# Kernel tuning notes

Measured on AMD Instinct MI355X. Metric: run time of the kernel, lower is better.

The kernel has to match this reference:

```python
import jax, jax.numpy as jnp
import numpy as np

N_HEAD = 16
N_FEAT = 1024
D_K = N_FEAT // N_HEAD


def rtt_half(x):
    x1, x2 = x[..., : x.shape[-1] // 2], x[..., x.shape[-1] // 2 :]
    return jnp.concatenate([-x2, x1], axis=-1)


def setup_inputs() -> dict:
    key = jax.random.key(0)
    ks = jax.random.split(key, 16)
    B, T, D = 4, 2048, N_FEAT
    inp = {
        "query": jax.random.normal(ks[0], (B, T, D), jnp.float32),
        "key": jax.random.normal(ks[1], (B, T, D), jnp.float32),
        "value": jax.random.normal(ks[2], (B, T, D), jnp.float32),
        "cos": jax.random.uniform(ks[3], (T, 1, D_K), jnp.float32),
        "sin": jax.random.uniform(ks[4], (T, 1, D_K), jnp.float32),
        "mask": jnp.zeros((B, T, T), jnp.bool_),
    }
    s = 1.0 / np.sqrt(D)
    inp["Wq"] = jax.random.uniform(ks[5], (D, D), jnp.float32, -s, s)
    inp["bq"] = jax.random.uniform(ks[6], (D,), jnp.float32, -s, s)
    inp["Wk"] = jax.random.uniform(ks[7], (D, D), jnp.float32, -s, s)
    inp["bk"] = jax.random.uniform(ks[8], (D,), jnp.float32, -s, s)
    inp["Wv"] = jax.random.uniform(ks[9], (D, D), jnp.float32, -s, s)
    inp["bv"] = jax.random.uniform(ks[10], (D,), jnp.float32, -s, s)
    inp["Wo"] = jax.random.uniform(ks[11], (D, D), jnp.float32, -s, s)
    inp["bo"] = jax.random.uniform(ks[12], (D,), jnp.float32, -s, s)
    return inp


def reference(query, key, value, cos, sin, mask, Wq, bq, Wk, bk, Wv, bv, Wo, bo):
    B, T, D = query.shape
    h, d_k = N_HEAD, D_K
    # QKV projections (torch Linear: x @ W.T + b), reshape to (B,T,h,d_k)
    q = (query @ Wq.T + bq).reshape(B, T, h, d_k)
    k = (key @ Wk.T + bk).reshape(B, T, h, d_k)
    v = (value @ Wv.T + bv).reshape(B, T, h, d_k)
    # RoPE: cos/sin sliced to T, broadcast (T,1,d_k) over (B,T,h,d_k)
    c, s = cos[:T], sin[:T]
    q = q * c + rtt_half(q) * s
    k = k * c + rtt_half(k) * s
    # attention scores (B,h,T,T)
    scores = jnp.einsum("bqhd,bkhd->bhqk", q, k) / np.sqrt(d_k).astype(jnp.float32)
    scores = jnp.where(mask[:, None, :, :], -jnp.inf, scores)
    attn = jax.nn.softmax(scores, axis=-1)
    out = jnp.einsum("bhqk,bkhd->bqhd", attn, v).reshape(B, T, D)
    return out @ Wo.T + bo
```

## Files before the change

kernel.cpp:

```cpp
#include <hip/hip_runtime.h>

#define B_SZ 4
#define T_SZ 2048
#define D_SZ 1024
#define H_SZ 16
#define DK_SZ 64
#define M_SZ (B_SZ * T_SZ)

typedef __attribute__((ext_vector_type(8))) short bf16x8;
typedef __attribute__((ext_vector_type(4))) short bf16x4;
typedef __attribute__((ext_vector_type(4))) float f32x4;

union fui { float f; unsigned u; };

static __device__ inline short f2bf(float x) {
    union { float f; unsigned u; } v; v.f = x;
    unsigned r = v.u + 0x7fff + ((v.u >> 16) & 1);
    return (short)(r >> 16);
}
static __device__ inline void split1(float f, short* h, short* l) {
    fui a; a.f = f;
    *h = (short)(a.u >> 16);
    fui t; t.u = a.u & 0xffff0000u;
    fui r; r.f = f - t.f;
    *l = (short)(r.u >> 16);
}

#define MFMA16(a, b, c) __builtin_amdgcn_mfma_f32_16x16x32_bf16((a), (b), (c), 0, 0, 0)

#define GLDS16(g, l) __builtin_amdgcn_global_load_lds(                        \
    (const __attribute__((address_space(1))) unsigned int*)(g),               \
    (__attribute__((address_space(3))) unsigned int*)(l), 16, 0, 0)

static __device__ inline void split8(float4 f0, float4 f1, bf16x8* hi, bf16x8* lo)
{
    fui a[8];
    a[0].f = f0.x; a[1].f = f0.y; a[2].f = f0.z; a[3].f = f0.w;
    a[4].f = f1.x; a[5].f = f1.y; a[6].f = f1.z; a[7].f = f1.w;
    union { unsigned w[4]; bf16x8 v; } H, L;
#pragma unroll
    for (int p = 0; p < 4; ++p)
        H.w[p] = __builtin_amdgcn_perm(a[2 * p + 1].u, a[2 * p].u, 0x07060302);
#pragma unroll
    for (int j = 0; j < 8; ++j) {
        fui t; t.u = a[j].u & 0xffff0000u;
        fui r; r.f = a[j].f - t.f;
        a[j].u = r.u;
    }
#pragma unroll
    for (int p = 0; p < 4; ++p)
        L.w[p] = __builtin_amdgcn_perm(a[2 * p + 1].u, a[2 * p].u, 0x07060302);
    *hi = H.v; *lo = L.v;
}

__global__ __launch_bounds__(256)
void wsplit_kernel(const float* __restrict__ W, short* __restrict__ Wh,
                   short* __restrict__ Wl)
{
    const int i = blockIdx.x * 256 + threadIdx.x;
    float4 f = ((const float4*)W)[i];
    fui a[4]; a[0].f = f.x; a[1].f = f.y; a[2].f = f.z; a[3].f = f.w;
    union { short s[4]; short4 v; } H, L;
#pragma unroll
    for (int j = 0; j < 4; ++j) {
        H.s[j] = (short)(a[j].u >> 16);
        fui t; t.u = a[j].u & 0xffff0000u;
        fui r; r.f = a[j].f - t.f;
        L.s[j] = (short)(r.u >> 16);
    }
    ((short4*)Wh)[i] = H.v;
    ((short4*)Wl)[i] = L.v;
}

__global__ __launch_bounds__(256)
void mask_flags_kernel(const unsigned char* __restrict__ mask, int* __restrict__ flags)
{
    const int f = blockIdx.x * 4 + (threadIdx.x >> 6);
    const int lane = threadIdx.x & 63;
    const int b = f >> 10, qt = (f >> 5) & 31, kt = f & 31;
    const unsigned char* base = mask + ((size_t)b * T_SZ + qt * 64) * T_SZ + kt * 64;
    bool nz = false;
#pragma unroll
    for (int i = 0; i < 4; ++i) {
        const int c = lane + 64 * i;
        const int row = c >> 2, off = (c & 3) * 16;
        uint4 v = *(const uint4*)(base + (size_t)row * T_SZ + off);
        nz |= ((v.x | v.y | v.z | v.w) != 0);
    }
    unsigned long long bal = __ballot(nz);
    if (lane == 0) flags[f] = (bal != 0) ? 1 : 0;
}

__global__ __launch_bounds__(256)
void qkv_mfma_kernel(const float* __restrict__ Aq, const float* __restrict__ Ak,
                     const float* __restrict__ Av,
                     const short* __restrict__ Wqh, const short* __restrict__ Wql,
                     const short* __restrict__ Wkh, const short* __restrict__ Wkl,
                     const short* __restrict__ Wvh, const short* __restrict__ Wvl,
                     const float* __restrict__ bq, const float* __restrict__ bk,
                     const float* __restrict__ bv,
                     const float* __restrict__ cosb, const float* __restrict__ sinb,
                     short* __restrict__ Qh, short* __restrict__ Ql,
                     short* __restrict__ Kh, short* __restrict__ Kl,
                     short* __restrict__ Vb)
{
    __shared__ __align__(16) short Whs[128 * 32];
    __shared__ __align__(16) short Wls[128 * 32];

    const int which = blockIdx.y >> 3;
    const int m0 = blockIdx.x * 128, n0 = (blockIdx.y & 7) * 128;
    const float* A  = (which == 0) ? Aq  : (which == 1) ? Ak  : Av;
    const short* Wh = (which == 0) ? Wqh : (which == 1) ? Wkh : Wvh;
    const short* Wl = (which == 0) ? Wql : (which == 1) ? Wkl : Wvl;
    const float* bias = (which == 0) ? bq : (which == 1) ? bk : bv;

    const int tid = threadIdx.x;
    const int wv = tid >> 6, lane = tid & 63;
    const int wm = wv >> 1, wn = wv & 1;
    const int l15 = lane & 15, quad = lane >> 4;

    f32x4 acc[4][4];
#pragma unroll
    for (int mt = 0; mt < 4; ++mt)
#pragma unroll
        for (int nt = 0; nt < 4; ++nt)
            acc[mt][nt] = (f32x4){0.f, 0.f, 0.f, 0.f};

    const short* whg = Wh + (size_t)(n0 + wv * 32 + (lane >> 2)) * D_SZ + (lane & 3) * 8;
    const short* wlg = Wl + (size_t)(n0 + wv * 32 + (lane >> 2)) * D_SZ + (lane & 3) * 8;
    short* whl0 = &Whs[wv * 1024];
    short* wll0 = &Wls[wv * 1024];

    const float* aB[4];
#pragma unroll
    for (int mt = 0; mt < 4; ++mt)
        aB[mt] = A + (size_t)(m0 + wm * 64 + mt * 16 + l15) * D_SZ + quad * 8;

    for (int k0 = 0; k0 < D_SZ; k0 += 32) {
        float4 af0[4], af1[4];
#pragma unroll
        for (int mt = 0; mt < 4; ++mt) {
            af0[mt] = *(const float4*)(aB[mt] + k0);
            af1[mt] = *(const float4*)(aB[mt] + k0 + 4);
        }
        __syncthreads();
        GLDS16(whg + k0,             whl0);
        GLDS16(whg + 16 * D_SZ + k0, whl0 + 512);
        GLDS16(wlg + k0,             wll0);
        GLDS16(wlg + 16 * D_SZ + k0, wll0 + 512);

        bf16x8 ah[4], al[4];
#pragma unroll
        for (int mt = 0; mt < 4; ++mt)
            split8(af0[mt], af1[mt], &ah[mt], &al[mt]);

        __syncthreads();

#pragma unroll
        for (int nt = 0; nt < 4; ++nt) {
            const int brow = (wn * 64 + nt * 16 + l15) * 32 + quad * 8;
            const bf16x8 bh = *(const bf16x8*)&Whs[brow];
            const bf16x8 bl = *(const bf16x8*)&Wls[brow];
#pragma unroll
            for (int mt = 0; mt < 4; ++mt) {
                acc[mt][nt] = MFMA16(ah[mt], bh, acc[mt][nt]);
                acc[mt][nt] = MFMA16(al[mt], bh, acc[mt][nt]);
                acc[mt][nt] = MFMA16(ah[mt], bl, acc[mt][nt]);
            }
        }
    }

    const int hh = ((blockIdx.y & 7) << 1) + wn;
    if (which < 2) {
        short* Hd = (which == 0) ? Qh : Kh;
        short* Ld = (which == 0) ? Ql : Kl;
        const float qscale = (which == 0) ? 0.125f : 1.0f;
#pragma unroll
        for (int mt = 0; mt < 4; ++mt)
#pragma unroll
            for (int p = 0; p < 2; ++p) {
                const int d1 = p * 16 + l15, d2 = d1 + 32;
                const int col1 = n0 + wn * 64 + d1;
                const float b1 = bias[col1], b2 = bias[col1 + 32];
#pragma unroll
                for (int r = 0; r < 4; ++r) {
                    const int m = m0 + wm * 64 + mt * 16 + quad * 4 + r;
                    const int bb = m >> 11, tg = m & (T_SZ - 1);
                    const float c1 = cosb[tg * 64 + d1], s1 = sinb[tg * 64 + d1];
                    const float c2 = cosb[tg * 64 + d2], s2 = sinb[tg * 64 + d2];
                    const float x1 = acc[mt][p][r] + b1;
                    const float x2 = acc[mt][p + 2][r] + b2;
                    const float y1 = (x1 * c1 - x2 * s1) * qscale;
                    const float y2 = (x2 * c2 + x1 * s2) * qscale;
                    const size_t base = (((size_t)(bb * H_SZ + hh)) * T_SZ + tg) * 64;
                    short h_, l_;
                    split1(y1, &h_, &l_); Hd[base + d1] = h_; Ld[base + d1] = l_;
                    split1(y2, &h_, &l_); Hd[base + d2] = h_; Ld[base + d2] = l_;
                }
            }
    } else {
#pragma unroll
        for (int nt = 0; nt < 4; ++nt) {
            const int d = nt * 16 + l15;
            const float bvv = bias[n0 + wn * 64 + d];
#pragma unroll
            for (int mt = 0; mt < 4; ++mt)
#pragma unroll
                for (int r = 0; r < 4; ++r) {
                    const int m = m0 + wm * 64 + mt * 16 + quad * 4 + r;
                    const int bb = m >> 11, tg = m & (T_SZ - 1);
                    Vb[(((size_t)(bb * H_SZ + hh)) * T_SZ + tg) * 64 + d] =
                        f2bf(acc[mt][nt][r] + bvv);
                }
        }
    }
}

__global__ __launch_bounds__(256)
void gemm_out_kernel(const float* __restrict__ A, const short* __restrict__ Wh,
                     const short* __restrict__ Wl, const float* __restrict__ bias,
                     float* __restrict__ C)
{
    __shared__ __align__(16) short Whs[128 * 32];
    __shared__ __align__(16) short Wls[128 * 32];

    const int m0 = blockIdx.x * 128, n0 = blockIdx.y * 128;
    const int tid = threadIdx.x;
    const int wv = tid >> 6, lane = tid & 63;
    const int wm = wv >> 1, wn = wv & 1;
    const int l15 = lane & 15, quad = lane >> 4;

    f32x4 acc[4][4];
#pragma unroll
    for (int mt = 0; mt < 4; ++mt)
#pragma unroll
        for (int nt = 0; nt < 4; ++nt)
            acc[mt][nt] = (f32x4){0.f, 0.f, 0.f, 0.f};

    const short* whg = Wh + (size_t)(n0 + wv * 32 + (lane >> 2)) * D_SZ + (lane & 3) * 8;
    const short* wlg = Wl + (size_t)(n0 + wv * 32 + (lane >> 2)) * D_SZ + (lane & 3) * 8;
    short* whl0 = &Whs[wv * 1024];
    short* wll0 = &Wls[wv * 1024];

    const float* aB[4];
#pragma unroll
    for (int mt = 0; mt < 4; ++mt)
        aB[mt] = A + (size_t)(m0 + wm * 64 + mt * 16 + l15) * D_SZ + quad * 8;

    for (int k0 = 0; k0 < D_SZ; k0 += 32) {
        float4 af0[4], af1[4];
#pragma unroll
        for (int mt = 0; mt < 4; ++mt) {
            af0[mt] = *(const float4*)(aB[mt] + k0);
            af1[mt] = *(const float4*)(aB[mt] + k0 + 4);
        }
        __syncthreads();
        GLDS16(whg + k0,             whl0);
        GLDS16(whg + 16 * D_SZ + k0, whl0 + 512);
        GLDS16(wlg + k0,             wll0);
        GLDS16(wlg + 16 * D_SZ + k0, wll0 + 512);

        bf16x8 ah[4], al[4];
#pragma unroll
        for (int mt = 0; mt < 4; ++mt)
            split8(af0[mt], af1[mt], &ah[mt], &al[mt]);

        __syncthreads();

#pragma unroll
        for (int nt = 0; nt < 4; ++nt) {
            const int brow = (wn * 64 + nt * 16 + l15) * 32 + quad * 8;
            const bf16x8 bh = *(const bf16x8*)&Whs[brow];
            const bf16x8 bl = *(const bf16x8*)&Wls[brow];
#pragma unroll
            for (int mt = 0; mt < 4; ++mt) {
                acc[mt][nt] = MFMA16(ah[mt], bh, acc[mt][nt]);
                acc[mt][nt] = MFMA16(al[mt], bh, acc[mt][nt]);
                acc[mt][nt] = MFMA16(ah[mt], bl, acc[mt][nt]);
            }
        }
    }

#pragma unroll
    for (int nt = 0; nt < 4; ++nt) {
        const int col = n0 + wn * 64 + nt * 16 + l15;
        const float bvv = bias[col];
#pragma unroll
        for (int mt = 0; mt < 4; ++mt)
#pragma unroll
            for (int r = 0; r < 4; ++r) {
                const int m = m0 + wm * 64 + mt * 16 + quad * 4 + r;
                C[(size_t)m * D_SZ + col] = acc[mt][nt][r] + bvv;
            }
    }
}

__global__ __launch_bounds__(256)
void attn_mfma_kernel(const short* __restrict__ Qhg, const short* __restrict__ Qlg,
                      const short* __restrict__ Khg, const short* __restrict__ Klg,
                      const short* __restrict__ Vg,
                      const unsigned char* __restrict__ mask,
                      const int* __restrict__ flags,
                      float* __restrict__ ob)
{
    __shared__ __align__(16) short Khs[64 * 72];
    __shared__ __align__(16) short Kls[64 * 72];
    __shared__ __align__(16) short Vt[64 * 72];
    __shared__ __align__(16) short Ps[4 * 16 * 72];

    const int bh = blockIdx.y;
    const int b = bh >> 4, h = bh & 15;
    const int q0 = blockIdx.x * 64;
    const int tid = threadIdx.x;
    const int wv = tid >> 6, lane = tid & 63;
    const int l15 = lane & 15, quad = lane >> 4;

    const short* qhp = Qhg + ((size_t)bh * T_SZ + q0 + wv * 16 + l15) * 64 + quad * 8;
    const short* qlp = Qlg + ((size_t)bh * T_SZ + q0 + wv * 16 + l15) * 64 + quad * 8;
    bf16x8 qh[2], ql[2];
#pragma unroll
    for (int s = 0; s < 2; ++s) {
        qh[s] = *(const bf16x8*)(qhp + 32 * s);
        ql[s] = *(const bf16x8*)(qlp + 32 * s);
    }

    f32x4 accO[4];
#pragma unroll
    for (int nt = 0; nt < 4; ++nt) accO[nt] = (f32x4){0.f, 0.f, 0.f, 0.f};
    float m_i[4], l_i[4];
#pragma unroll
    for (int r = 0; r < 4; ++r) { m_i[r] = -1e30f; l_i[r] = 0.f; }

    const short* khb = Khg + (size_t)bh * T_SZ * 64;
    const short* klb = Klg + (size_t)bh * T_SZ * 64;
    const short* vb  = Vg  + (size_t)bh * T_SZ * 64;
    const unsigned char* mbase = mask + ((size_t)b * T_SZ + q0) * T_SZ;
    const int* frow = flags + ((size_t)b * 32 + blockIdx.x) * 32;

    const short* kgp[4];
    short*       kld[4];
#pragma unroll
    for (int jj = 0; jj < 4; ++jj) {
        const int cc = tid + 256 * (jj & 1);
        const int row = cc >> 3, off = (cc & 7) * 8;
        kgp[jj] = ((jj < 2) ? khb : klb) + (size_t)row * 64 + off;
        kld[jj] = ((jj < 2) ? Khs : Kls) + row * 72 + off;
    }
    const int vt0 = (tid & 15) * 4, vd0 = (tid >> 4) * 4;
    const short* vgp[4];
#pragma unroll
    for (int i = 0; i < 4; ++i)
        vgp[i] = vb + (size_t)(vt0 + i) * 64 + vd0;
    short* pw = &Ps[wv * 16 * 72];

    bf16x8 kst[4];
    uint2  rv[4];
#pragma unroll
    for (int jj = 0; jj < 4; ++jj) kst[jj] = *(const bf16x8*)(kgp[jj]);
#pragma unroll
    for (int i = 0; i < 4; ++i)    rv[i]   = *(const uint2*)(vgp[i]);

    for (int kti = 0; kti < 32; ++kti) {
        const int kt = kti * 64;
        __syncthreads();
#pragma unroll
        for (int jj = 0; jj < 4; ++jj)
            *(bf16x8*)kld[jj] = kst[jj];
#pragma unroll
        for (int c = 0; c < 4; ++c) {
            const int k = c >> 1;
            const unsigned sel = (c & 1) ? 0x07060302u : 0x05040100u;
            const unsigned lo0 = k ? rv[0].y : rv[0].x;
            const unsigned lo1 = k ? rv[1].y : rv[1].x;
            const unsigned lo2 = k ? rv[2].y : rv[2].x;
            const unsigned lo3 = k ? rv[3].y : rv[3].x;
            uint2 o;
            o.x = __builtin_amdgcn_perm(lo1, lo0, sel);
            o.y = __builtin_amdgcn_perm(lo3, lo2, sel);
            *(uint2*)&Vt[(vd0 + c) * 72 + vt0] = o;
        }
        if (kti < 31) {
            const size_t adv = (size_t)(kt + 64) * 64;
#pragma unroll
            for (int jj = 0; jj < 4; ++jj)
                kst[jj] = *(const bf16x8*)(kgp[jj] + adv);
#pragma unroll
            for (int i = 0; i < 4; ++i)
                rv[i] = *(const uint2*)(vgp[i] + adv);
        }
        __syncthreads();

        f32x4 accS[4];
        __builtin_amdgcn_s_setprio(1);
#pragma unroll
        for (int nt = 0; nt < 4; ++nt) {
            f32x4 acc = (f32x4){0.f, 0.f, 0.f, 0.f};
#pragma unroll
            for (int s = 0; s < 2; ++s) {
                const bf16x8 kh = *(const bf16x8*)&Khs[(nt * 16 + l15) * 72 + 32 * s + quad * 8];
                const bf16x8 kl = *(const bf16x8*)&Kls[(nt * 16 + l15) * 72 + 32 * s + quad * 8];
                acc = MFMA16(qh[s], kh, acc);
                acc = MFMA16(ql[s], kh, acc);
                acc = MFMA16(qh[s], kl, acc);
            }
            accS[nt] = acc;
        }
        __builtin_amdgcn_s_setprio(0);

        float sv[4][4];
        if (frow[kti]) {
#pragma unroll
            for (int nt = 0; nt < 4; ++nt)
#pragma unroll
                for (int r = 0; r < 4; ++r) {
                    const unsigned char mb =
                        mbase[(size_t)(wv * 16 + quad * 4 + r) * T_SZ + kt + nt * 16 + l15];
                    sv[nt][r] = mb ? -1e30f : accS[nt][r];
                }
        } else {
#pragma unroll
            for (int nt = 0; nt < 4; ++nt)
#pragma unroll
                for (int r = 0; r < 4; ++r)
                    sv[nt][r] = accS[nt][r];
        }

        float rmax[4];
#pragma unroll
        for (int r = 0; r < 4; ++r)
            rmax[r] = fmaxf(fmaxf(sv[0][r], sv[1][r]), fmaxf(sv[2][r], sv[3][r]));
#pragma unroll
        for (int off = 1; off < 16; off <<= 1)
#pragma unroll
            for (int r = 0; r < 4; ++r)
                rmax[r] = fmaxf(rmax[r], __shfl_xor(rmax[r], off, 64));

        float alpha[4];
#pragma unroll
        for (int r = 0; r < 4; ++r) {
            const float mnew = fmaxf(m_i[r], rmax[r]);
            alpha[r] = __expf(m_i[r] - mnew);
            m_i[r] = mnew;
        }
        float lsum[4] = {0.f, 0.f, 0.f, 0.f};
#pragma unroll
        for (int nt = 0; nt < 4; ++nt)
#pragma unroll
            for (int r = 0; r < 4; ++r) {
                const float p = __expf(sv[nt][r] - m_i[r]);
                sv[nt][r] = p;
                lsum[r] += p;
            }
#pragma unroll
        for (int r = 0; r < 4; ++r)
            l_i[r] = l_i[r] * alpha[r] + lsum[r];

#pragma unroll
        for (int nt = 0; nt < 4; ++nt)
#pragma unroll
            for (int r = 0; r < 4; ++r) {
                fui u; u.f = sv[nt][r];
                pw[(quad * 4 + r) * 72 + nt * 16 + l15] = (short)((u.u + 0x8000u) >> 16);
            }

#pragma unroll
        for (int nt = 0; nt < 4; ++nt)
#pragma unroll
            for (int r = 0; r < 4; ++r)
                accO[nt][r] *= alpha[r];

        bf16x8 pa[2];
#pragma unroll
        for (int s = 0; s < 2; ++s)
            pa[s] = *(const bf16x8*)&pw[l15 * 72 + 32 * s + quad * 8];
        __builtin_amdgcn_s_setprio(1);
#pragma unroll
        for (int nt = 0; nt < 4; ++nt)
#pragma unroll
            for (int s = 0; s < 2; ++s) {
                const bf16x8 vf = *(const bf16x8*)&Vt[(nt * 16 + l15) * 72 + 32 * s + quad * 8];
                accO[nt] = MFMA16(pa[s], vf, accO[nt]);
            }
        __builtin_amdgcn_s_setprio(0);
    }

#pragma unroll
    for (int off = 1; off < 16; off <<= 1)
#pragma unroll
        for (int r = 0; r < 4; ++r)
            l_i[r] += __shfl_xor(l_i[r], off, 64);

#pragma unroll
    for (int r = 0; r < 4; ++r) {
        const float inv = 1.f / l_i[r];
        const int t = q0 + wv * 16 + quad * 4 + r;
        float* orow = ob + ((size_t)(b * T_SZ + t)) * D_SZ + h * DK_SZ;
#pragma unroll
        for (int nt = 0; nt < 4; ++nt)
            orow[nt * 16 + l15] = accO[nt][r] * inv;
    }
}

extern "C" void kernel_launch(void* const* d_in, const int* in_sizes, int n_in,
                              void* d_out, int out_size, void* d_ws, size_t ws_size,
                              hipStream_t stream)
{
    const float* query = (const float*)d_in[0];
    const float* key   = (const float*)d_in[1];
    const float* value = (const float*)d_in[2];
    const float* cosb  = (const float*)d_in[3];
    const float* sinb  = (const float*)d_in[4];
    const unsigned char* mask = (const unsigned char*)d_in[5];
    const float* Wq = (const float*)d_in[6];
    const float* bq = (const float*)d_in[7];
    const float* Wk = (const float*)d_in[8];
    const float* bk = (const float*)d_in[9];
    const float* Wv = (const float*)d_in[10];
    const float* bv = (const float*)d_in[11];
    const float* Wo = (const float*)d_in[12];
    const float* bo = (const float*)d_in[13];
    float* out = (float*)d_out;

    short* sp = (short*)d_ws;
    const size_t eb = (size_t)B_SZ * H_SZ * T_SZ * DK_SZ;
    short* Qh = sp;          short* Ql = sp + eb;
    short* Kh = sp + 2 * eb; short* Kl = sp + 3 * eb;
    short* Vb = sp + 4 * eb;
    float* abuf = (float*)(sp + 5 * eb);
    short* wsp = (short*)(abuf + eb);
    const size_t wlen = (size_t)D_SZ * D_SZ;
    short* wqh = wsp;            short* wql = wsp + wlen;
    short* wkh = wsp + 2 * wlen; short* wkl = wsp + 3 * wlen;
    short* wvh = wsp + 4 * wlen; short* wvl = wsp + 5 * wlen;
    short* woh = wsp + 6 * wlen; short* wol = wsp + 7 * wlen;
    int* flags = (int*)(wsp + 8 * wlen);

    const int wsBlocks = (int)(wlen / 4 / 256);
    wsplit_kernel<<<wsBlocks, 256, 0, stream>>>(Wq, wqh, wql);
    wsplit_kernel<<<wsBlocks, 256, 0, stream>>>(Wk, wkh, wkl);
    wsplit_kernel<<<wsBlocks, 256, 0, stream>>>(Wv, wvh, wvl);
    wsplit_kernel<<<wsBlocks, 256, 0, stream>>>(Wo, woh, wol);

    mask_flags_kernel<<<1024, 256, 0, stream>>>(mask, flags);

    qkv_mfma_kernel<<<dim3(M_SZ / 128, 24), 256, 0, stream>>>(
        query, key, value, wqh, wql, wkh, wkl, wvh, wvl,
        bq, bk, bv, cosb, sinb, Qh, Ql, Kh, Kl, Vb);

    attn_mfma_kernel<<<dim3(T_SZ / 64, B_SZ * H_SZ), 256, 0, stream>>>(
        Qh, Ql, Kh, Kl, Vb, mask, flags, abuf);

    gemm_out_kernel<<<dim3(M_SZ / 128, D_SZ / 128), 256, 0, stream>>>(
        abuf, woh, wol, bo, out);
}
```

Baseline: 728.6 us.

## Pre-split GEMM activations to bf16 hi/lo and stage them via LDS

After: 665.5 us. 8.7% less time.

```diff
diff --git a/kernel.cpp b/kernel.cpp
--- a/kernel.cpp
+++ b/kernel.cpp
@@ -31,27 +31,6 @@
 #define GLDS16(g, l) __builtin_amdgcn_global_load_lds(                        \
     (const __attribute__((address_space(1))) unsigned int*)(g),               \
     (__attribute__((address_space(3))) unsigned int*)(l), 16, 0, 0)
-
-static __device__ inline void split8(float4 f0, float4 f1, bf16x8* hi, bf16x8* lo)
-{
-    fui a[8];
-    a[0].f = f0.x; a[1].f = f0.y; a[2].f = f0.z; a[3].f = f0.w;
-    a[4].f = f1.x; a[5].f = f1.y; a[6].f = f1.z; a[7].f = f1.w;
-    union { unsigned w[4]; bf16x8 v; } H, L;
-#pragma unroll
-    for (int p = 0; p < 4; ++p)
-        H.w[p] = __builtin_amdgcn_perm(a[2 * p + 1].u, a[2 * p].u, 0x07060302);
-#pragma unroll
-    for (int j = 0; j < 8; ++j) {
-        fui t; t.u = a[j].u & 0xffff0000u;
-        fui r; r.f = a[j].f - t.f;
-        a[j].u = r.u;
-    }
-#pragma unroll
-    for (int p = 0; p < 4; ++p)
-        L.w[p] = __builtin_amdgcn_perm(a[2 * p + 1].u, a[2 * p].u, 0x07060302);
-    *hi = H.v; *lo = L.v;
-}
 
 __global__ __launch_bounds__(256)
 void wsplit_kernel(const float* __restrict__ W, short* __restrict__ Wh,
@@ -92,28 +71,19 @@
 }
 
 __global__ __launch_bounds__(256)
-void qkv_mfma_kernel(const float* __restrict__ Aq, const float* __restrict__ Ak,
-                     const float* __restrict__ Av,
-                     const short* __restrict__ Wqh, const short* __restrict__ Wql,
-                     const short* __restrict__ Wkh, const short* __restrict__ Wkl,
-                     const short* __restrict__ Wvh, const short* __restrict__ Wvl,
-                     const float* __restrict__ bq, const float* __restrict__ bk,
-                     const float* __restrict__ bv,
+void qkv_mfma_kernel(const short* __restrict__ Ah, const short* __restrict__ Al,
+                     const short* __restrict__ Wh, const short* __restrict__ Wl,
+                     const float* __restrict__ bias,
                      const float* __restrict__ cosb, const float* __restrict__ sinb,
-                     short* __restrict__ Qh, short* __restrict__ Ql,
-                     short* __restrict__ Kh, short* __restrict__ Kl,
-                     short* __restrict__ Vb)
+                     short* __restrict__ Hd, short* __restrict__ Ld,
+                     short* __restrict__ Vb, const int which)
 {
+    __shared__ __align__(16) short Ahs[128 * 32];
+    __shared__ __align__(16) short Als[128 * 32];
     __shared__ __align__(16) short Whs[128 * 32];
     __shared__ __align__(16) short Wls[128 * 32];
 
-    const int which = blockIdx.y >> 3;
-    const int m0 = blockIdx.x * 128, n0 = (blockIdx.y & 7) * 128;
-    const float* A  = (which == 0) ? Aq  : (which == 1) ? Ak  : Av;
-    const short* Wh = (which == 0) ? Wqh : (which == 1) ? Wkh : Wvh;
-    const short* Wl = (which == 0) ? Wql : (which == 1) ? Wkl : Wvl;
-    const float* bias = (which == 0) ? bq : (which == 1) ? bk : bv;
-
+    const int m0 = blockIdx.x * 128, n0 = blockIdx.y * 128;
     const int tid = threadIdx.x;
     const int wv = tid >> 6, lane = tid & 63;
     const int wm = wv >> 1, wn = wv & 1;
@@ -126,36 +96,36 @@
         for (int nt = 0; nt < 4; ++nt)
             acc[mt][nt] = (f32x4){0.f, 0.f, 0.f, 0.f};
 
-    const short* whg = Wh + (size_t)(n0 + wv * 32 + (lane >> 2)) * D_SZ + (lane & 3) * 8;
-    const short* wlg = Wl + (size_t)(n0 + wv * 32 + (lane >> 2)) * D_SZ + (lane & 3) * 8;
-    short* whl0 = &Whs[wv * 1024];
-    short* wll0 = &Wls[wv * 1024];
-
-    const float* aB[4];
-#pragma unroll
-    for (int mt = 0; mt < 4; ++mt)
-        aB[mt] = A + (size_t)(m0 + wm * 64 + mt * 16 + l15) * D_SZ + quad * 8;
+    const size_t aoff = (size_t)(m0 + wv * 32 + (lane >> 2)) * D_SZ + (lane & 3) * 8;
+    const size_t woff = (size_t)(n0 + wv * 32 + (lane >> 2)) * D_SZ + (lane & 3) * 8;
+    const short* ahg = Ah + aoff;
+    const short* alg = Al + aoff;
+    const short* whg = Wh + woff;
+    const short* wlg = Wl + woff;
+    short* ah0 = &Ahs[wv * 1024];
+    short* al0 = &Als[wv * 1024];
+    short* wh0 = &Whs[wv * 1024];
+    short* wl0 = &Wls[wv * 1024];
 
     for (int k0 = 0; k0 < D_SZ; k0 += 32) {
-        float4 af0[4], af1[4];
+        __syncthreads();
+        GLDS16(ahg + k0,             ah0);
+        GLDS16(ahg + 16 * D_SZ + k0, ah0 + 512);
+        GLDS16(alg + k0,             al0);
+        GLDS16(alg + 16 * D_SZ + k0, al0 + 512);
+        GLDS16(whg + k0,             wh0);
+        GLDS16(whg + 16 * D_SZ + k0, wh0 + 512);
+        GLDS16(wlg + k0,             wl0);
+        GLDS16(wlg + 16 * D_SZ + k0, wl0 + 512);
+        __syncthreads();
+
+        bf16x8 ah[4], al[4];
 #pragma unroll
         for (int mt = 0; mt < 4; ++mt) {
-            af0[mt] = *(const float4*)(aB[mt] + k0);
-            af1[mt] = *(const float4*)(aB[mt] + k0 + 4);
-        }
-        __syncthreads();
-        GLDS16(whg + k0,             whl0);
-        GLDS16(whg + 16 * D_SZ + k0, whl0 + 512);
-        GLDS16(wlg + k0,             wll0);
-        GLDS16(wlg + 16 * D_SZ + k0, wll0 + 512);
-
-        bf16x8 ah[4], al[4];
-#pragma unroll
-        for (int mt = 0; mt < 4; ++mt)
-            split8(af0[mt], af1[mt], &ah[mt], &al[mt]);
-
-        __syncthreads();
-
+            const int arow = (wm * 64 + mt * 16 + l15) * 32 + quad * 8;
+            ah[mt] = *(const bf16x8*)&Ahs[arow];
+            al[mt] = *(const bf16x8*)&Als[arow];
+        }
 #pragma unroll
         for (int nt = 0; nt < 4; ++nt) {
             const int brow = (wn * 64 + nt * 16 + l15) * 32 + quad * 8;
@@ -170,10 +140,8 @@
         }
     }
 
-    const int hh = ((blockIdx.y & 7) << 1) + wn;
+    const int hh = (blockIdx.y << 1) + wn;
     if (which < 2) {
-        short* Hd = (which == 0) ? Qh : Kh;
-        short* Ld = (which == 0) ? Ql : Kl;
         const float qscale = (which == 0) ? 0.125f : 1.0f;
 #pragma unroll
         for (int mt = 0; mt < 4; ++mt)
@@ -217,10 +185,12 @@
 }
 
 __global__ __launch_bounds__(256)
-void gemm_out_kernel(const float* __restrict__ A, const short* __restrict__ Wh,
-                     const short* __restrict__ Wl, const float* __restrict__ bias,
-                     float* __restrict__ C)
+void gemm_out_kernel(const short* __restrict__ Ah, const short* __restrict__ Al,
+                     const short* __restrict__ Wh, const short* __restrict__ Wl,
+                     const float* __restrict__ bias, float* __restrict__ C)
 {
+    __shared__ __align__(16) short Ahs[128 * 32];
+    __shared__ __align__(16) short Als[128 * 32];
     __shared__ __align__(16) short Whs[128 * 32];
     __shared__ __align__(16) short Wls[128 * 32];
 
@@ -237,36 +207,36 @@
         for (int nt = 0; nt < 4; ++nt)
             acc[mt][nt] = (f32x4){0.f, 0.f, 0.f, 0.f};
 
-    const short* whg = Wh + (size_t)(n0 + wv * 32 + (lane >> 2)) * D_SZ + (lane & 3) * 8;
-    const short* wlg = Wl + (size_t)(n0 + wv * 32 + (lane >> 2)) * D_SZ + (lane & 3) * 8;
-    short* whl0 = &Whs[wv * 1024];
-    short* wll0 = &Wls[wv * 1024];
-
-    const float* aB[4];
-#pragma unroll
-    for (int mt = 0; mt < 4; ++mt)
-        aB[mt] = A + (size_t)(m0 + wm * 64 + mt * 16 + l15) * D_SZ + quad * 8;
+    const size_t aoff = (size_t)(m0 + wv * 32 + (lane >> 2)) * D_SZ + (lane & 3) * 8;
+    const size_t woff = (size_t)(n0 + wv * 32 + (lane >> 2)) * D_SZ + (lane & 3) * 8;
+    const short* ahg = Ah + aoff;
+    const short* alg = Al + aoff;
+    const short* whg = Wh + woff;
+    const short* wlg = Wl + woff;
+    short* ah0 = &Ahs[wv * 1024];
+    short* al0 = &Als[wv * 1024];
+    short* wh0 = &Whs[wv * 1024];
+    short* wl0 = &Wls[wv * 1024];
 
     for (int k0 = 0; k0 < D_SZ; k0 += 32) {
-        float4 af0[4], af1[4];
+        __syncthreads();
+        GLDS16(ahg + k0,             ah0);
+        GLDS16(ahg + 16 * D_SZ + k0, ah0 + 512);
+        GLDS16(alg + k0,             al0);
+        GLDS16(alg + 16 * D_SZ + k0, al0 + 512);
+        GLDS16(whg + k0,             wh0);
+        GLDS16(whg + 16 * D_SZ + k0, wh0 + 512);
+        GLDS16(wlg + k0,             wl0);
+        GLDS16(wlg + 16 * D_SZ + k0, wl0 + 512);
+        __syncthreads();
+
+        bf16x8 ah[4], al[4];
 #pragma unroll
         for (int mt = 0; mt < 4; ++mt) {
-            af0[mt] = *(const float4*)(aB[mt] + k0);
-            af1[mt] = *(const float4*)(aB[mt] + k0 + 4);
-        }
-        __syncthreads();
-        GLDS16(whg + k0,             whl0);
-        GLDS16(whg + 16 * D_SZ + k0, whl0 + 512);
-        GLDS16(wlg + k0,             wll0);
-        GLDS16(wlg + 16 * D_SZ + k0, wll0 + 512);
-
-        bf16x8 ah[4], al[4];
-#pragma unroll
-        for (int mt = 0; mt < 4; ++mt)
-            split8(af0[mt], af1[mt], &ah[mt], &al[mt]);
-
-        __syncthreads();
-
+            const int arow = (wm * 64 + mt * 16 + l15) * 32 + quad * 8;
+            ah[mt] = *(const bf16x8*)&Ahs[arow];
+            al[mt] = *(const bf16x8*)&Als[arow];
+        }
 #pragma unroll
         for (int nt = 0; nt < 4; ++nt) {
             const int brow = (wn * 64 + nt * 16 + l15) * 32 + quad * 8;
@@ -301,7 +271,7 @@
                       const short* __restrict__ Vg,
                       const unsigned char* __restrict__ mask,
                       const int* __restrict__ flags,
-                      float* __restrict__ ob)
+                      short* __restrict__ Oh, short* __restrict__ Ol)
 {
     __shared__ __align__(16) short Khs[64 * 72];
     __shared__ __align__(16) short Kls[64 * 72];
@@ -494,10 +464,14 @@
     for (int r = 0; r < 4; ++r) {
         const float inv = 1.f / l_i[r];
         const int t = q0 + wv * 16 + quad * 4 + r;
-        float* orow = ob + ((size_t)(b * T_SZ + t)) * D_SZ + h * DK_SZ;
-#pragma unroll
-        for (int nt = 0; nt < 4; ++nt)
-            orow[nt * 16 + l15] = accO[nt][r] * inv;
+        const size_t base = ((size_t)(b * T_SZ + t)) * D_SZ + h * DK_SZ;
+#pragma unroll
+        for (int nt = 0; nt < 4; ++nt) {
+            short h_, l_;
+            split1(accO[nt][r] * inv, &h_, &l_);
+            Oh[base + nt * 16 + l15] = h_;
+            Ol[base + nt * 16 + l15] = l_;
+        }
     }
 }
 
@@ -526,8 +500,8 @@
     short* Qh = sp;          short* Ql = sp + eb;
     short* Kh = sp + 2 * eb; short* Kl = sp + 3 * eb;
     short* Vb = sp + 4 * eb;
-    float* abuf = (float*)(sp + 5 * eb);
-    short* wsp = (short*)(abuf + eb);
+    short* Xh = sp + 5 * eb; short* Xl = sp + 6 * eb;
+    short* wsp = sp + 7 * eb;
     const size_t wlen = (size_t)D_SZ * D_SZ;
     short* wqh = wsp;            short* wql = wsp + wlen;
     short* wkh = wsp + 2 * wlen; short* wkl = wsp + 3 * wlen;
@@ -536,6 +510,7 @@
     int* flags = (int*)(wsp + 8 * wlen);
 
     const int wsBlocks = (int)(wlen / 4 / 256);
+    const int aBlocks  = (int)((size_t)M_SZ * D_SZ / 4 / 256);
     wsplit_kernel<<<wsBlocks, 256, 0, stream>>>(Wq, wqh, wql);
     wsplit_kernel<<<wsBlocks, 256, 0, stream>>>(Wk, wkh, wkl);
     wsplit_kernel<<<wsBlocks, 256, 0, stream>>>(Wv, wvh, wvl);
@@ -543,13 +518,19 @@
 
     mask_flags_kernel<<<1024, 256, 0, stream>>>(mask, flags);
 
-    qkv_mfma_kernel<<<dim3(M_SZ / 128, 24), 256, 0, stream>>>(
-        query, key, value, wqh, wql, wkh, wkl, wvh, wvl,
-        bq, bk, bv, cosb, sinb, Qh, Ql, Kh, Kl, Vb);
+    wsplit_kernel<<<aBlocks, 256, 0, stream>>>(query, Xh, Xl);
+    qkv_mfma_kernel<<<dim3(M_SZ / 128, 8), 256, 0, stream>>>(
+        Xh, Xl, wqh, wql, bq, cosb, sinb, Qh, Ql, Vb, 0);
+    wsplit_kernel<<<aBlocks, 256, 0, stream>>>(key, Xh, Xl);
+    qkv_mfma_kernel<<<dim3(M_SZ / 128, 8), 256, 0, stream>>>(
+        Xh, Xl, wkh, wkl, bk, cosb, sinb, Kh, Kl, Vb, 1);
+    wsplit_kernel<<<aBlocks, 256, 0, stream>>>(value, Xh, Xl);
+    qkv_mfma_kernel<<<dim3(M_SZ / 128, 8), 256, 0, stream>>>(
+        Xh, Xl, wvh, wvl, bv, cosb, sinb, Qh, Ql, Vb, 2);
 
     attn_mfma_kernel<<<dim3(T_SZ / 64, B_SZ * H_SZ), 256, 0, stream>>>(
-        Qh, Ql, Kh, Kl, Vb, mask, flags, abuf);
+        Qh, Ql, Kh, Kl, Vb, mask, flags, Xh, Xl);
 
     gemm_out_kernel<<<dim3(M_SZ / 128, D_SZ / 128), 256, 0, stream>>>(
-        abuf, woh, wol, bo, out);
-}
+        Xh, Xl, woh, wol, bo, out);
+}
```
